# Kernel tuning notes

Hardware: AMD Instinct MI355X
Metric: run time of the kernel (lower is better)

Reference implementation:

```python
import jax, jax.numpy as jnp
import numpy as np

N_NODES = 100000


def _sage_conv(x, src, dst, Wl, b, Wr):
    """PyG SAGEConv with mean aggregation: lin_l(mean_{j->i} x_j) + lin_r(x_i)."""
    msg = x[src]  # [E, d] gather of source-node features
    s = jax.ops.segment_sum(msg, dst, num_segments=N_NODES)  # [N, d]
    deg = jax.ops.segment_sum(jnp.ones_like(dst, dtype=x.dtype), dst,
                              num_segments=N_NODES)  # [N]
    mean = s / jnp.maximum(deg, 1.0)[:, None]  # nodes with no in-edges -> 0
    return mean @ Wl.T + b + x @ Wr.T


def setup_inputs() -> dict:
    key = jax.random.key(0)
    ks = jax.random.split(key, 12)
    in_f, h_f, out_f = 64, 64, 32
    E_half = 800000
    x = jax.random.normal(ks[0], (N_NODES, in_f), dtype=jnp.float32)
    edge_index1 = jax.random.randint(ks[1], (2, E_half), 0, N_NODES, dtype=jnp.int64)
    edge_weight1 = jax.random.uniform(ks[2], (E_half,), dtype=jnp.float32)
    edge_index2 = jax.random.randint(ks[3], (2, E_half), 0, N_NODES, dtype=jnp.int64)
    edge_weight2 = jax.random.uniform(ks[4], (E_half,), dtype=jnp.float32)
    s1 = 1.0 / np.sqrt(in_f)
    s2 = 1.0 / np.sqrt(h_f)
    W1l = jax.random.uniform(ks[5], (h_f, in_f), minval=-s1, maxval=s1, dtype=jnp.float32)
    b1 = jax.random.uniform(ks[6], (h_f,), minval=-s1, maxval=s1, dtype=jnp.float32)
    W1r = jax.random.uniform(ks[7], (h_f, in_f), minval=-s1, maxval=s1, dtype=jnp.float32)
    W2l = jax.random.uniform(ks[8], (out_f, h_f), minval=-s2, maxval=s2, dtype=jnp.float32)
    b2 = jax.random.uniform(ks[9], (out_f,), minval=-s2, maxval=s2, dtype=jnp.float32)
    W2r = jax.random.uniform(ks[10], (out_f, h_f), minval=-s2, maxval=s2, dtype=jnp.float32)
    return {"x": x, "edge_index1": edge_index1, "edge_weight1": edge_weight1,
            "edge_index2": edge_index2, "edge_weight2": edge_weight2,
            "W1l": W1l, "b1": b1, "W1r": W1r, "W2l": W2l, "b2": b2, "W2r": W2r}


def reference(x, edge_index1, edge_weight1, edge_index2, edge_weight2,
              W1l, b1, W1r, W2l, b2, W2r):
    # concat adjacency lists (edge_weight is concatenated but unused by SAGEConv)
    edge_index = jnp.concatenate([edge_index1, edge_index2], axis=-1)
    _edge_weight = jnp.concatenate([edge_weight1, edge_weight2], axis=-1)  # unused
    src, dst = edge_index[0], edge_index[1]
    # F.dropout with training=False -> identity (eval-mode reference)
    h = _sage_conv(x, src, dst, W1l, b1, W1r)
    h = jax.nn.relu(h)
    out = _sage_conv(h, src, dst, W2l, b2, W2r)
    return out
```

## Files before the change

kernel.cpp:

```cpp
#include <hip/hip_runtime.h>


constexpr int N_NODES = 100000;
constexpr int E_HALF  = 800000;
constexpr int E_TOT   = 2 * E_HALF;
constexpr int CAP     = 64;
constexpr int OVF_CAP = 4096;
constexpr int NB      = 200;
constexpr int NPB     = 500;
constexpr int BCAP    = 12288;
constexpr int EPB_A   = 2048;
constexpr int EPT_A   = EPB_A / 256;

typedef short  s16x8 __attribute__((ext_vector_type(8)));
typedef float  f32x4 __attribute__((ext_vector_type(4)));
typedef unsigned short u16;

__device__ inline float bf(u16 u) { return __uint_as_float(((unsigned)u) << 16); }
__device__ inline u16 f2bf(float v) {
    unsigned b = __float_as_uint(v);
    b += 0x7FFFu + ((b >> 16) & 1u);
    return (u16)(b >> 16);
}
__device__ inline void acc4(float* s, uint2 v) {
    s[0] += __uint_as_float(v.x << 16);
    s[1] += __uint_as_float(v.x & 0xFFFF0000u);
    s[2] += __uint_as_float(v.y << 16);
    s[3] += __uint_as_float(v.y & 0xFFFF0000u);
}

__global__ __launch_bounds__(256) void binA_kernel(
    const int* __restrict__ ei1, const int* __restrict__ ei2,
    uint2* __restrict__ barr, int* __restrict__ bcur,
    int* __restrict__ ovfA_cnt, int* __restrict__ ovfA)
{
    __shared__ int   hist[NB], base[NB], cur[NB], lofs[NB];
    __shared__ int   scan[256];
    __shared__ int   aux[EPB_A];
    __shared__ uint2 staged[EPB_A];
    int tid = threadIdx.x;
    for (int t = tid; t < NB; t += 256) { hist[t] = 0; cur[t] = 0; }
    __syncthreads();

    int e0 = blockIdx.x * EPB_A;
    uint2 myE[EPT_A];
    int   myB[EPT_A];
    #pragma unroll
    for (int k = 0; k < EPT_A; k++) {
        int e = e0 + k * 256 + tid;
        myB[k] = -1;
        if (e < E_TOT) {
            const int* ei = (e < E_HALF) ? ei1 : ei2;
            int ee = (e < E_HALF) ? e : e - E_HALF;
            int dst = ei[E_HALF + ee];
            int src = ei[ee];
            myE[k] = make_uint2((unsigned)src, (unsigned)dst);
            myB[k] = dst / NPB;
            atomicAdd(&hist[myB[k]], 1);
        }
    }
    __syncthreads();

    int v = (tid < NB) ? hist[tid] : 0;
    scan[tid] = v;
    __syncthreads();
    #pragma unroll
    for (int off = 1; off < 256; off <<= 1) {
        int u = (tid >= off) ? scan[tid - off] : 0;
        __syncthreads();
        scan[tid] += u;
        __syncthreads();
    }
    if (tid < NB) lofs[tid] = scan[tid] - v;
    if (tid < NB) base[tid] = atomicAdd(&bcur[tid], hist[tid]);
    __syncthreads();

    #pragma unroll
    for (int k = 0; k < EPT_A; k++) {
        int b = myB[k];
        if (b < 0) continue;
        int rank = atomicAdd(&cur[b], 1);
        int p    = lofs[b] + rank;
        int gpos = base[b] + rank;
        if (gpos < BCAP) {
            staged[p] = myE[k];
            aux[p]    = b * BCAP + gpos;
        } else {
            aux[p] = -1;
            int o = atomicAdd(ovfA_cnt, 1);
            if (o < OVF_CAP) {
                ovfA[2 * o] = (int)myE[k].x; ovfA[2 * o + 1] = (int)myE[k].y;
            }
        }
    }
    __syncthreads();

    int tot = scan[255];
    for (int i = tid; i < tot; i += 256) {
        int a = aux[i];
        if (a >= 0) barr[a] = staged[i];
    }
}

__global__ __launch_bounds__(1024) void binB_kernel(
    const uint2* __restrict__ barr, const int* __restrict__ bcur,
    const int* __restrict__ ovfA_cnt, const int* __restrict__ ovfA,
    int* __restrict__ cnt, int* __restrict__ slots,
    int* __restrict__ ovfB_cnt, int* __restrict__ ovfB)
{
    __shared__ int lcnt[NPB];
    int tid = threadIdx.x, b = blockIdx.x;
    for (int t = tid; t < NPB; t += 1024) lcnt[t] = 0;
    __syncthreads();
    int nE = bcur[b]; if (nE > BCAP) nE = BCAP;
    int dbase = b * NPB;
    for (int i = tid; i < nE; i += 1024) {
        uint2 e = barr[b * BCAP + i];
        int dst = (int)e.y;
        int pos = atomicAdd(&lcnt[dst - dbase], 1);
        if (pos < CAP) {
            slots[dst * CAP + pos] = (int)e.x;
        } else {
            int o = atomicAdd(ovfB_cnt, 1);
            if (o < OVF_CAP) { ovfB[2 * o] = (int)e.x; ovfB[2 * o + 1] = dst; }
        }
    }
    __syncthreads();
    int nOA = *ovfA_cnt; if (nOA > OVF_CAP) nOA = OVF_CAP;
    for (int t = tid; t < nOA; t += 1024) {
        int src = ovfA[2 * t], dst = ovfA[2 * t + 1];
        if (dst >= dbase && dst < dbase + NPB) {
            int pos = atomicAdd(&lcnt[dst - dbase], 1);
            if (pos < CAP) {
                slots[dst * CAP + pos] = src;
            } else {
                int o = atomicAdd(ovfB_cnt, 1);
                if (o < OVF_CAP) { ovfB[2 * o] = src; ovfB[2 * o + 1] = dst; }
            }
        }
    }
    __syncthreads();
    for (int t = tid; t < NPB; t += 1024) {
        int n = dbase + t;
        if (n < N_NODES) cnt[n] = lcnt[t];
    }
}

__global__ __launch_bounds__(256) void prep_kernel(
    const float* __restrict__ x, u16* __restrict__ xb,
    const float* __restrict__ W1l, const float* __restrict__ W1r,
    const float* __restrict__ W2l, const float* __restrict__ W2r,
    short* __restrict__ B1hi, short* __restrict__ B1lo,
    short* __restrict__ B2hi, short* __restrict__ B2lo,
    int* __restrict__ zinit)
{
    int blk = blockIdx.x;
    if (blk == 6298) {
        for (int t = threadIdx.x; t < 320; t += 256) zinit[t] = 0;
        return;
    }
    if (blk < 6250) {
        int i = blk * 256 + threadIdx.x;
        float4 v = ((const float4*)x)[i];
        ushort4 rr;
        rr.x = f2bf(v.x); rr.y = f2bf(v.y); rr.z = f2bf(v.z); rr.w = f2bf(v.w);
        ((ushort4*)xb)[i] = rr;
        return;
    }
    int i = (blk - 6250) * 256 + threadIdx.x;
    float v; short* ph; short* pl; int idx;
    if (i < 64 * 128) {
        int o = i >> 7, k = i & 127;
        v = (k < 64) ? W1l[o * 64 + k] : W1r[o * 64 + (k - 64)];
        ph = B1hi; pl = B1lo; idx = i;
    } else {
        int j = i - 64 * 128;
        int o = j >> 6, k = j & 63;
        v = (o < 32) ? W2l[o * 64 + k] : W2r[(o - 32) * 64 + k];
        ph = B2hi; pl = B2lo; idx = j;
    }
    unsigned b  = __float_as_uint(v);
    float    hf = __uint_as_float(b & 0xFFFF0000u);
    float    r  = v - hf;
    ph[idx] = (short)(b >> 16);
    pl[idx] = (short)(__float_as_uint(r) >> 16);
}

__device__ inline void split8(float4 v0, float4 v1, s16x8& hi, s16x8& lo) {
    float vs[8] = {v0.x, v0.y, v0.z, v0.w, v1.x, v1.y, v1.z, v1.w};
    s16x8 h, l;
    #pragma unroll
    for (int j = 0; j < 8; j++) {
        unsigned b  = __float_as_uint(vs[j]);
        float    hf = __uint_as_float(b & 0xFFFF0000u);
        float    r  = vs[j] - hf;
        h[j] = (short)(b >> 16);
        l[j] = (short)(__float_as_uint(r) >> 16);
    }
    hi = h; lo = l;
}

template <int MT>
__global__ __launch_bounds__(256) void gather_gemm1_kernel(
    const u16*  __restrict__ xb,
    const float* __restrict__ x,
    const int*  __restrict__ cnt,
    const int*  __restrict__ slots,
    const int*  __restrict__ ovfB_cnt, const int* __restrict__ ovfB,
    const short* __restrict__ Bhi, const short* __restrict__ Blo,
    const float* __restrict__ bias, u16* __restrict__ hb)
{
    constexpr int RPW = MT * 16;
    __shared__ float ldsA[4][RPW][66];
    const int widx = threadIdx.x >> 6;
    const int lane = threadIdx.x & 63;
    const int m0   = (blockIdx.x * 4 + widx) * RPW;
    const int r = lane >> 4;
    const int c = lane & 15;

    int pdA, pdB, psvA, psvB;
    {
        int nA = m0, nB = m0 + 1;
        pdA  = (nA < N_NODES) ? cnt[nA] : 0;
        pdB  = (nB < N_NODES) ? cnt[nB] : 0;
        psvA = (nA < N_NODES) ? slots[nA * CAP + lane] : 0;
        psvB = (nB < N_NODES) ? slots[nB * CAP + lane] : 0;
    }
    #pragma unroll 1
    for (int j = 0; j < RPW; j += 2) {
        const int dA = pdA, dB = pdB;
        const int rsvA = psvA, rsvB = psvB;
        if (j + 2 < RPW) {
            int nA = m0 + j + 2, nB = m0 + j + 3;
            pdA  = (nA < N_NODES) ? cnt[nA] : 0;
            pdB  = (nB < N_NODES) ? cnt[nB] : 0;
            psvA = (nA < N_NODES) ? slots[nA * CAP + lane] : 0;
            psvB = (nB < N_NODES) ? slots[nB * CAP + lane] : 0;
        }
        const int cA = dA < CAP ? dA : CAP;
        const int cB = dB < CAP ? dB : CAP;
        const int svA = (lane < cA) ? rsvA : 0;
        const int svB = (lane < cB) ? rsvB : 0;
        float sA[16], sB[16];
        #pragma unroll
        for (int k = 0; k < 16; k++) { sA[k] = 0.f; sB[k] = 0.f; }
        const int cM = cA > cB ? cA : cB;
        for (int i = 0; i < cM; i += 16) {
            const int i0 = i + r, i1 = i + 4 + r, i2 = i + 8 + r, i3 = i + 12 + r;
            int tA0 = __shfl(svA, i0), tA1 = __shfl(svA, i1),
                tA2 = __shfl(svA, i2), tA3 = __shfl(svA, i3);
            int tB0 = __shfl(svB, i0), tB1 = __shfl(svB, i1),
                tB2 = __shfl(svB, i2), tB3 = __shfl(svB, i3);
            uint2 vA0 = make_uint2(0u, 0u), vA1 = vA0, vA2 = vA0, vA3 = vA0;
            uint2 vB0 = vA0, vB1 = vA0, vB2 = vA0, vB3 = vA0;
            if (i0 < cA) vA0 = *(const uint2*)&xb[tA0 * 64 + c * 4];
            if (i1 < cA) vA1 = *(const uint2*)&xb[tA1 * 64 + c * 4];
            if (i2 < cA) vA2 = *(const uint2*)&xb[tA2 * 64 + c * 4];
            if (i3 < cA) vA3 = *(const uint2*)&xb[tA3 * 64 + c * 4];
            if (i0 < cB) vB0 = *(const uint2*)&xb[tB0 * 64 + c * 4];
            if (i1 < cB) vB1 = *(const uint2*)&xb[tB1 * 64 + c * 4];
            if (i2 < cB) vB2 = *(const uint2*)&xb[tB2 * 64 + c * 4];
            if (i3 < cB) vB3 = *(const uint2*)&xb[tB3 * 64 + c * 4];
            acc4(&sA[0], vA0); acc4(&sA[4], vA1);
            acc4(&sA[8], vA2); acc4(&sA[12], vA3);
            acc4(&sB[0], vB0); acc4(&sB[4], vB1);
            acc4(&sB[8], vB2); acc4(&sB[12], vB3);
        }
        #pragma unroll
        for (int k = 0; k < 4; k++) {
            float fA = sA[k] + sA[k + 4] + sA[k + 8] + sA[k + 12];
            float fB = sB[k] + sB[k + 4] + sB[k + 8] + sB[k + 12];
            fA += __shfl_xor(fA, 16); fA += __shfl_xor(fA, 32);
            fB += __shfl_xor(fB, 16); fB += __shfl_xor(fB, 32);
            sA[k] = fA; sB[k] = fB;
        }
        if (r == 0) {
            const float rdA = 1.0f / fmaxf((float)dA, 1.0f);
            const float rdB = 1.0f / fmaxf((float)dB, 1.0f);
            float2* pA = (float2*)&ldsA[widx][j][c * 4];
            float2* pB = (float2*)&ldsA[widx][j + 1][c * 4];
            pA[0] = make_float2(sA[0] * rdA, sA[1] * rdA);
            pA[1] = make_float2(sA[2] * rdA, sA[3] * rdA);
            pB[0] = make_float2(sB[0] * rdB, sB[1] * rdB);
            pB[1] = make_float2(sB[2] * rdB, sB[3] * rdB);
        }
    }
    __syncthreads();

    {
        int nOv = *ovfB_cnt; if (nOv > OVF_CAP) nOv = OVF_CAP;
        for (int t = 0; t < nOv; ++t) {
            int src = ovfB[2 * t], dst = ovfB[2 * t + 1];
            if (dst >= m0 && dst < m0 + RPW && dst < N_NODES) {
                float rd = 1.0f / fmaxf((float)cnt[dst], 1.0f);
                ldsA[widx][dst - m0][lane] += bf(xb[src * 64 + lane]) * rd;
            }
        }
    }
    __syncthreads();

    f32x4 acc[MT][4];
    #pragma unroll
    for (int mt = 0; mt < MT; mt++)
        #pragma unroll
        for (int nt = 0; nt < 4; nt++) acc[mt][nt] = (f32x4)0.0f;

    #pragma unroll
    for (int half = 0; half < 2; half++) {
        #pragma unroll
        for (int sub = 0; sub < 2; sub++) {
            const int kf = sub * 32 + r * 8;
            const int kc = half * 64 + kf;
            s16x8 ahi[MT], alo[MT];
            #pragma unroll
            for (int mt = 0; mt < MT; mt++) {
                if (half == 0) {
                    const float2* p = (const float2*)&ldsA[widx][mt * 16 + c][kf];
                    float2 q0 = p[0], q1 = p[1], q2 = p[2], q3 = p[3];
                    split8(make_float4(q0.x, q0.y, q1.x, q1.y),
                           make_float4(q2.x, q2.y, q3.x, q3.y),
                           ahi[mt], alo[mt]);
                } else {
                    int row = m0 + mt * 16 + c;
                    row = row < N_NODES ? row : N_NODES - 1;
                    const float4* p = (const float4*)&x[row * 64 + kf];
                    split8(p[0], p[1], ahi[mt], alo[mt]);
                }
            }
            #pragma unroll
            for (int nt = 0; nt < 4; nt++) {
                const int n = nt * 16 + c;
                s16x8 bh = *(const s16x8*)&Bhi[n * 128 + kc];
                s16x8 bl = *(const s16x8*)&Blo[n * 128 + kc];
                #pragma unroll
                for (int mt = 0; mt < MT; mt++) {
                    acc[mt][nt] = __builtin_amdgcn_mfma_f32_16x16x32_bf16(ahi[mt], bh, acc[mt][nt], 0, 0, 0);
                    acc[mt][nt] = __builtin_amdgcn_mfma_f32_16x16x32_bf16(alo[mt], bh, acc[mt][nt], 0, 0, 0);
                    acc[mt][nt] = __builtin_amdgcn_mfma_f32_16x16x32_bf16(ahi[mt], bl, acc[mt][nt], 0, 0, 0);
                    acc[mt][nt] = __builtin_amdgcn_mfma_f32_16x16x32_bf16(alo[mt], bl, acc[mt][nt], 0, 0, 0);
                }
            }
        }
    }
    #pragma unroll
    for (int nt = 0; nt < 4; nt++) {
        float bv = bias[nt * 16 + c];
        #pragma unroll
        for (int mt = 0; mt < MT; mt++)
            #pragma unroll
            for (int rr = 0; rr < 4; rr++) {
                int row = m0 + mt * 16 + r * 4 + rr;
                if (row < N_NODES)
                    hb[row * 64 + nt * 16 + c] =
                        f2bf(fmaxf(acc[mt][nt][rr] + bv, 0.0f));
            }
    }
}

template <int MT>
__global__ __launch_bounds__(256) void gemm2_kernel(
    const u16* __restrict__ hb,
    const short* __restrict__ Bhi, const short* __restrict__ Blo,
    const float* __restrict__ b2,
    u16* __restrict__ y2b, float* __restrict__ z)
{
    int wave = (blockIdx.x * 256 + threadIdx.x) >> 6;
    int lane = threadIdx.x & 63;
    int m0   = wave * (MT * 16);
    if (m0 >= N_NODES) return;
    int quad = lane >> 4, l16 = lane & 15;

    f32x4 acc[MT][4];
    #pragma unroll
    for (int mt = 0; mt < MT; mt++)
        #pragma unroll
        for (int nt = 0; nt < 4; nt++) acc[mt][nt] = (f32x4)0.0f;

    #pragma unroll
    for (int sub = 0; sub < 2; sub++) {
        int kf = sub * 32 + quad * 8;
        s16x8 a[MT];
        #pragma unroll
        for (int mt = 0; mt < MT; mt++) {
            int row = m0 + mt * 16 + l16;
            row = row < N_NODES ? row : N_NODES - 1;
            a[mt] = *(const s16x8*)&hb[row * 64 + kf];
        }
        #pragma unroll
        for (int nt = 0; nt < 4; nt++) {
            int n = nt * 16 + l16;
            s16x8 bh = *(const s16x8*)&Bhi[n * 64 + kf];
            s16x8 bl = *(const s16x8*)&Blo[n * 64 + kf];
            #pragma unroll
            for (int mt = 0; mt < MT; mt++) {
                acc[mt][nt] = __builtin_amdgcn_mfma_f32_16x16x32_bf16(a[mt], bh, acc[mt][nt], 0, 0, 0);
                acc[mt][nt] = __builtin_amdgcn_mfma_f32_16x16x32_bf16(a[mt], bl, acc[mt][nt], 0, 0, 0);
            }
        }
    }
    #pragma unroll
    for (int nt = 0; nt < 4; nt++) {
        bool  isz = nt >= 2;
        int   col = (isz ? nt - 2 : nt) * 16 + l16;
        float bv  = isz ? b2[col] : 0.0f;
        #pragma unroll
        for (int mt = 0; mt < MT; mt++)
            #pragma unroll
            for (int r = 0; r < 4; r++) {
                int row = m0 + mt * 16 + quad * 4 + r;
                if (row < N_NODES) {
                    float v = acc[mt][nt][r] + bv;
                    if (isz) z[row * 32 + col] = v;
                    else     y2b[row * 32 + col] = f2bf(v);
                }
            }
    }
}

__global__ __launch_bounds__(256) void gather_mean32_kernel(
    const u16*  __restrict__ y2b,
    const float* __restrict__ z,
    const int*  __restrict__ cnt,
    const int*  __restrict__ slots,
    const int*  __restrict__ ovfB_cnt, const int* __restrict__ ovfB,
    float*      __restrict__ out)
{
    int node = blockIdx.x * 4 + (threadIdx.x >> 6);
    int lane = threadIdx.x & 63;
    int r    = lane >> 3;
    int c    = lane & 7;
    if (node >= N_NODES) return;
    int nOv = *ovfB_cnt; if (nOv > OVF_CAP) nOv = OVF_CAP;
    int cdeg = cnt[node];
    int cc   = cdeg < CAP ? cdeg : CAP;
    int slotv = (lane < cc) ? slots[node * CAP + lane] : 0;
    float s[16];
    #pragma unroll
    for (int k = 0; k < 16; k++) s[k] = 0.f;
    for (int i = 0; i < cc; i += 32) {
        int i0 = i + r, i1 = i + 8 + r, i2 = i + 16 + r, i3 = i + 24 + r;
        int t0 = __shfl(slotv, i0), t1 = __shfl(slotv, i1),
            t2 = __shfl(slotv, i2), t3 = __shfl(slotv, i3);
        uint2 v0 = make_uint2(0u, 0u), v1 = v0, v2 = v0, v3 = v0;
        if (i0 < cc) v0 = *(const uint2*)&y2b[t0 * 32 + c * 4];
        if (i1 < cc) v1 = *(const uint2*)&y2b[t1 * 32 + c * 4];
        if (i2 < cc) v2 = *(const uint2*)&y2b[t2 * 32 + c * 4];
        if (i3 < cc) v3 = *(const uint2*)&y2b[t3 * 32 + c * 4];
        acc4(&s[0], v0); acc4(&s[4], v1); acc4(&s[8], v2); acc4(&s[12], v3);
    }
    #pragma unroll
    for (int k = 0; k < 4; k++) {
        float f = s[k] + s[k + 4] + s[k + 8] + s[k + 12];
        f += __shfl_xor(f, 8); f += __shfl_xor(f, 16); f += __shfl_xor(f, 32);
        s[k] = f;
    }
    for (int t = 0; t < nOv; ++t) {
        int src = ovfB[2 * t], dst = ovfB[2 * t + 1];
        if (dst == node) {
            uint2 v = *(const uint2*)&y2b[src * 32 + c * 4];
            s[0] += __uint_as_float(v.x << 16);
            s[1] += __uint_as_float(v.x & 0xFFFF0000u);
            s[2] += __uint_as_float(v.y << 16);
            s[3] += __uint_as_float(v.y & 0xFFFF0000u);
        }
    }
    if (r == 0) {
        float rd = 1.0f / fmaxf((float)cdeg, 1.0f);
        float4 zz = *(const float4*)&z[node * 32 + c * 4];
        *(float4*)&out[node * 32 + c * 4] = make_float4(
            s[0] * rd + zz.x, s[1] * rd + zz.y,
            s[2] * rd + zz.z, s[3] * rd + zz.w);
    }
}

extern "C" void kernel_launch(void* const* d_in, const int* in_sizes, int n_in,
                              void* d_out, int out_size, void* d_ws, size_t ws_size,
                              hipStream_t stream) {
    const float* x   = (const float*)d_in[0];
    const int*   ei1 = (const int*)d_in[1];
    const int*   ei2 = (const int*)d_in[3];
    const float* W1l = (const float*)d_in[5];
    const float* b1  = (const float*)d_in[6];
    const float* W1r = (const float*)d_in[7];
    const float* W2l = (const float*)d_in[8];
    const float* b2  = (const float*)d_in[9];
    const float* W2r = (const float*)d_in[10];
    float* out = (float*)d_out;

    const size_t off_misc  = 400128;
    const size_t off_ovfAc = off_misc + 0;
    const size_t off_ovfBc = off_misc + 4;
    const size_t off_bcur  = off_misc + 256;
    const size_t off_ovfA  = off_misc + 1280;
    const size_t off_ovfB  = off_misc + 1280 + 8 * OVF_CAP;
    const size_t off_slots = 467200;
    const size_t off_m     = off_slots + (size_t)N_NODES * CAP * 4;
    const size_t off_h     = off_m + (size_t)N_NODES * 64 * 4;
    const size_t off_hb    = off_h + (size_t)N_NODES * 64 * 2;
    const size_t off_B1hi  = off_h + (size_t)N_NODES * 64 * 4;
    const size_t off_B1lo  = off_B1hi + 64 * 128 * 2;
    const size_t off_B2hi  = off_B1lo + 64 * 128 * 2;
    const size_t off_B2lo  = off_B2hi + 64 * 64 * 2;

    char*  ws     = (char*)d_ws;
    int*   cnt    = (int*)(ws + 0);
    int*   ovfA_c = (int*)(ws + off_ovfAc);
    int*   ovfB_c = (int*)(ws + off_ovfBc);
    int*   bcur   = (int*)(ws + off_bcur);
    int*   ovfA   = (int*)(ws + off_ovfA);
    int*   ovfB   = (int*)(ws + off_ovfB);
    int*   slots  = (int*)(ws + off_slots);
    uint2* barr   = (uint2*)(ws + off_m);
    u16*   xb     = (u16*)(ws + off_h);
    u16*   hb     = (u16*)(ws + off_hb);
    float* z      = (float*)(ws + off_m);
    u16*   y2b    = (u16*)(ws + off_m + (size_t)N_NODES * 32 * 4);
    short* B1hi   = (short*)(ws + off_B1hi);
    short* B1lo   = (short*)(ws + off_B1lo);
    short* B2hi   = (short*)(ws + off_B2hi);
    short* B2lo   = (short*)(ws + off_B2lo);

    prep_kernel<<<6250 + 48 + 1, 256, 0, stream>>>(
        x, xb, W1l, W1r, W2l, W2r, B1hi, B1lo, B2hi, B2lo,
        (int*)(ws + off_misc));

    binA_kernel<<<(E_TOT + EPB_A - 1) / EPB_A, 256, 0, stream>>>(
        ei1, ei2, barr, bcur, ovfA_c, ovfA);
    binB_kernel<<<NB, 1024, 0, stream>>>(
        barr, bcur, ovfA_c, ovfA, cnt, slots, ovfB_c, ovfB);

    {
        int waves  = (N_NODES + 31) / 32;
        int blocks = (waves + 3) / 4;
        gather_gemm1_kernel<2><<<blocks, 256, 0, stream>>>(
            xb, x, cnt, slots, ovfB_c, ovfB, B1hi, B1lo, b1, hb);
    }

    {
        int waves = (N_NODES + 63) / 64;
        gemm2_kernel<4><<<(waves + 3) / 4, 256, 0, stream>>>(
            hb, B2hi, B2lo, b2, y2b, z);
    }
    gather_mean32_kernel<<<N_NODES / 4, 256, 0, stream>>>(
        y2b, z, cnt, slots, ovfB_c, ovfB, out);
}
```

Measured before the change: 236.9 us.

## Fuse layer-2 GEMM into gather-GEMM1, fold bf16 conversion into binning kernel

Removes the separate prep and gemm2 kernels. The x-to-bf16 conversion now runs as extra blocks of the binning kernel, and the weight hi/lo bf16 split is done inline from fp32 weights inside the GEMMs. The hidden activations stay in LDS, so the second linear layer runs in the same kernel without writing hb to global memory. Counter zeroing moves to a memset. This saves launches and an HBM round-trip of h, at the cost of recomputing the weight splits in every wave and extra LDS syncs.

```diff
diff --git a/kernel.cpp b/kernel.cpp
--- a/kernel.cpp
+++ b/kernel.cpp
@@ -11,6 +11,8 @@
 constexpr int BCAP    = 12288;
 constexpr int EPB_A   = 2048;
 constexpr int EPT_A   = EPB_A / 256;
+constexpr int BINA_BLKS = (E_TOT + EPB_A - 1) / EPB_A;
+constexpr int CONV_BLKS = N_NODES * 64 / 4 / 256;
 
 typedef short  s16x8 __attribute__((ext_vector_type(8)));
 typedef float  f32x4 __attribute__((ext_vector_type(4)));
@@ -29,8 +31,23 @@
     s[3] += __uint_as_float(v.y & 0xFFFF0000u);
 }
 
+__device__ inline void split8(float4 v0, float4 v1, s16x8& hi, s16x8& lo) {
+    float vs[8] = {v0.x, v0.y, v0.z, v0.w, v1.x, v1.y, v1.z, v1.w};
+    s16x8 h, l;
+    #pragma unroll
+    for (int j = 0; j < 8; j++) {
+        unsigned b  = __float_as_uint(vs[j]);
+        float    hf = __uint_as_float(b & 0xFFFF0000u);
+        float    r  = vs[j] - hf;
+        h[j] = (short)(b >> 16);
+        l[j] = (short)(__float_as_uint(r) >> 16);
+    }
+    hi = h; lo = l;
+}
+
 __global__ __launch_bounds__(256) void binA_kernel(
     const int* __restrict__ ei1, const int* __restrict__ ei2,
+    const float* __restrict__ x, u16* __restrict__ xb,
     uint2* __restrict__ barr, int* __restrict__ bcur,
     int* __restrict__ ovfA_cnt, int* __restrict__ ovfA)
 {
@@ -39,6 +56,16 @@
     __shared__ int   aux[EPB_A];
     __shared__ uint2 staged[EPB_A];
     int tid = threadIdx.x;
+
+    if (blockIdx.x >= BINA_BLKS) {
+        int i = (blockIdx.x - BINA_BLKS) * 256 + tid;
+        float4 v = ((const float4*)x)[i];
+        ushort4 rr;
+        rr.x = f2bf(v.x); rr.y = f2bf(v.y); rr.z = f2bf(v.z); rr.w = f2bf(v.w);
+        ((ushort4*)xb)[i] = rr;
+        return;
+    }
+
     for (int t = tid; t < NB; t += 256) { hist[t] = 0; cur[t] = 0; }
     __syncthreads();
 
@@ -146,69 +173,18 @@
     }
 }
 
-__global__ __launch_bounds__(256) void prep_kernel(
-    const float* __restrict__ x, u16* __restrict__ xb,
-    const float* __restrict__ W1l, const float* __restrict__ W1r,
-    const float* __restrict__ W2l, const float* __restrict__ W2r,
-    short* __restrict__ B1hi, short* __restrict__ B1lo,
-    short* __restrict__ B2hi, short* __restrict__ B2lo,
-    int* __restrict__ zinit)
-{
-    int blk = blockIdx.x;
-    if (blk == 6298) {
-        for (int t = threadIdx.x; t < 320; t += 256) zinit[t] = 0;
-        return;
-    }
-    if (blk < 6250) {
-        int i = blk * 256 + threadIdx.x;
-        float4 v = ((const float4*)x)[i];
-        ushort4 rr;
-        rr.x = f2bf(v.x); rr.y = f2bf(v.y); rr.z = f2bf(v.z); rr.w = f2bf(v.w);
-        ((ushort4*)xb)[i] = rr;
-        return;
-    }
-    int i = (blk - 6250) * 256 + threadIdx.x;
-    float v; short* ph; short* pl; int idx;
-    if (i < 64 * 128) {
-        int o = i >> 7, k = i & 127;
-        v = (k < 64) ? W1l[o * 64 + k] : W1r[o * 64 + (k - 64)];
-        ph = B1hi; pl = B1lo; idx = i;
-    } else {
-        int j = i - 64 * 128;
-        int o = j >> 6, k = j & 63;
-        v = (o < 32) ? W2l[o * 64 + k] : W2r[(o - 32) * 64 + k];
-        ph = B2hi; pl = B2lo; idx = j;
-    }
-    unsigned b  = __float_as_uint(v);
-    float    hf = __uint_as_float(b & 0xFFFF0000u);
-    float    r  = v - hf;
-    ph[idx] = (short)(b >> 16);
-    pl[idx] = (short)(__float_as_uint(r) >> 16);
-}
-
-__device__ inline void split8(float4 v0, float4 v1, s16x8& hi, s16x8& lo) {
-    float vs[8] = {v0.x, v0.y, v0.z, v0.w, v1.x, v1.y, v1.z, v1.w};
-    s16x8 h, l;
-    #pragma unroll
-    for (int j = 0; j < 8; j++) {
-        unsigned b  = __float_as_uint(vs[j]);
-        float    hf = __uint_as_float(b & 0xFFFF0000u);
-        float    r  = vs[j] - hf;
-        h[j] = (short)(b >> 16);
-        l[j] = (short)(__float_as_uint(r) >> 16);
-    }
-    hi = h; lo = l;
-}
-
 template <int MT>
-__global__ __launch_bounds__(256) void gather_gemm1_kernel(
+__global__ __launch_bounds__(256) void gather_gemm12_kernel(
     const u16*  __restrict__ xb,
     const float* __restrict__ x,
     const int*  __restrict__ cnt,
     const int*  __restrict__ slots,
     const int*  __restrict__ ovfB_cnt, const int* __restrict__ ovfB,
-    const short* __restrict__ Bhi, const short* __restrict__ Blo,
-    const float* __restrict__ bias, u16* __restrict__ hb)
+    const float* __restrict__ W1l, const float* __restrict__ W1r,
+    const float* __restrict__ b1,
+    const float* __restrict__ W2l, const float* __restrict__ W2r,
+    const float* __restrict__ b2,
+    u16* __restrict__ y2b, float* __restrict__ z)
 {
     constexpr int RPW = MT * 16;
     __shared__ float ldsA[4][RPW][66];
@@ -217,6 +193,7 @@
     const int m0   = (blockIdx.x * 4 + widx) * RPW;
     const int r = lane >> 4;
     const int c = lane & 15;
+    u16* hbT = (u16*)&ldsA[widx][0][0];
 
     int pdA, pdB, psvA, psvB;
     {
@@ -247,10 +224,10 @@
         const int cM = cA > cB ? cA : cB;
         for (int i = 0; i < cM; i += 16) {
             const int i0 = i + r, i1 = i + 4 + r, i2 = i + 8 + r, i3 = i + 12 + r;
-            int tA0 = __shfl(svA, i0), tA1 = __shfl(svA, i1),
-                tA2 = __shfl(svA, i2), tA3 = __shfl(svA, i3);
-            int tB0 = __shfl(svB, i0), tB1 = __shfl(svB, i1),
-                tB2 = __shfl(svB, i2), tB3 = __shfl(svB, i3);
+            int tA0 = __shfl(svA, i0 & 63), tA1 = __shfl(svA, i1 & 63),
+                tA2 = __shfl(svA, i2 & 63), tA3 = __shfl(svA, i3 & 63);
+            int tB0 = __shfl(svB, i0 & 63), tB1 = __shfl(svB, i1 & 63),
+                tB2 = __shfl(svB, i2 & 63), tB3 = __shfl(svB, i3 & 63);
             uint2 vA0 = make_uint2(0u, 0u), vA1 = vA0, vA2 = vA0, vA3 = vA0;
             uint2 vB0 = vA0, vB1 = vA0, vB2 = vA0, vB3 = vA0;
             if (i0 < cA) vA0 = *(const uint2*)&xb[tA0 * 64 + c * 4];
@@ -261,9 +238,9 @@
             if (i1 < cB) vB1 = *(const uint2*)&xb[tB1 * 64 + c * 4];
             if (i2 < cB) vB2 = *(const uint2*)&xb[tB2 * 64 + c * 4];
             if (i3 < cB) vB3 = *(const uint2*)&xb[tB3 * 64 + c * 4];
-            acc4(&sA[0], vA0); acc4(&sA[4], vA1);
+            acc4(&sA[0], vA0); acc4(&sA[4],  vA1);
             acc4(&sA[8], vA2); acc4(&sA[12], vA3);
-            acc4(&sB[0], vB0); acc4(&sB[4], vB1);
+            acc4(&sB[0], vB0); acc4(&sB[4],  vB1);
             acc4(&sB[8], vB2); acc4(&sB[12], vB3);
         }
         #pragma unroll
@@ -307,10 +284,10 @@
 
     #pragma unroll
     for (int half = 0; half < 2; half++) {
+        const float* W1 = half ? W1r : W1l;
         #pragma unroll
         for (int sub = 0; sub < 2; sub++) {
             const int kf = sub * 32 + r * 8;
-            const int kc = half * 64 + kf;
             s16x8 ahi[MT], alo[MT];
             #pragma unroll
             for (int mt = 0; mt < MT; mt++) {
@@ -330,8 +307,9 @@
             #pragma unroll
             for (int nt = 0; nt < 4; nt++) {
                 const int n = nt * 16 + c;
-                s16x8 bh = *(const s16x8*)&Bhi[n * 128 + kc];
-                s16x8 bl = *(const s16x8*)&Blo[n * 128 + kc];
+                const float4* wp = (const float4*)&W1[n * 64 + kf];
+                s16x8 bh, bl;
+                split8(wp[0], wp[1], bh, bl);
                 #pragma unroll
                 for (int mt = 0; mt < MT; mt++) {
                     acc[mt][nt] = __builtin_amdgcn_mfma_f32_16x16x32_bf16(ahi[mt], bh, acc[mt][nt], 0, 0, 0);
@@ -342,74 +320,62 @@
             }
         }
     }
+    __syncthreads();
+
     #pragma unroll
     for (int nt = 0; nt < 4; nt++) {
-        float bv = bias[nt * 16 + c];
+        float bv = b1[nt * 16 + c];
+        #pragma unroll
+        for (int mt = 0; mt < MT; mt++)
+            #pragma unroll
+            for (int rr = 0; rr < 4; rr++) {
+                int lrow = mt * 16 + r * 4 + rr;
+                u16 hv = (m0 + lrow < N_NODES)
+                           ? f2bf(fmaxf(acc[mt][nt][rr] + bv, 0.0f)) : (u16)0;
+                hbT[lrow * 72 + nt * 16 + c] = hv;
+            }
+    }
+    __syncthreads();
+
+    f32x4 acc2[MT][4];
+    #pragma unroll
+    for (int mt = 0; mt < MT; mt++)
+        #pragma unroll
+        for (int nt = 0; nt < 4; nt++) acc2[mt][nt] = (f32x4)0.0f;
+
+    #pragma unroll
+    for (int sub = 0; sub < 2; sub++) {
+        const int kf = sub * 32 + r * 8;
+        s16x8 a2[MT];
+        #pragma unroll
+        for (int mt = 0; mt < MT; mt++)
+            a2[mt] = *(const s16x8*)&hbT[(mt * 16 + c) * 72 + kf];
+        #pragma unroll
+        for (int nt = 0; nt < 4; nt++) {
+            const int n = nt * 16 + c;
+            const float4* wp = (n < 32) ? (const float4*)&W2l[n * 64 + kf]
+                                        : (const float4*)&W2r[(n - 32) * 64 + kf];
+            s16x8 bh, bl;
+            split8(wp[0], wp[1], bh, bl);
+            #pragma unroll
+            for (int mt = 0; mt < MT; mt++) {
+                acc2[mt][nt] = __builtin_amdgcn_mfma_f32_16x16x32_bf16(a2[mt], bh, acc2[mt][nt], 0, 0, 0);
+                acc2[mt][nt] = __builtin_amdgcn_mfma_f32_16x16x32_bf16(a2[mt], bl, acc2[mt][nt], 0, 0, 0);
+            }
+        }
+    }
+    #pragma unroll
+    for (int nt = 0; nt < 4; nt++) {
+        bool  isz = nt >= 2;
+        int   col = (isz ? nt - 2 : nt) * 16 + c;
+        float bv  = isz ? b2[col] : 0.0f;
         #pragma unroll
         for (int mt = 0; mt < MT; mt++)
             #pragma unroll
             for (int rr = 0; rr < 4; rr++) {
                 int row = m0 + mt * 16 + r * 4 + rr;
-                if (row < N_NODES)
-                    hb[row * 64 + nt * 16 + c] =
-                        f2bf(fmaxf(acc[mt][nt][rr] + bv, 0.0f));
-            }
-    }
-}
-
-template <int MT>
-__global__ __launch_bounds__(256) void gemm2_kernel(
-    const u16* __restrict__ hb,
-    const short* __restrict__ Bhi, const short* __restrict__ Blo,
-    const float* __restrict__ b2,
-    u16* __restrict__ y2b, float* __restrict__ z)
-{
-    int wave = (blockIdx.x * 256 + threadIdx.x) >> 6;
-    int lane = threadIdx.x & 63;
-    int m0   = wave * (MT * 16);
-    if (m0 >= N_NODES) return;
-    int quad = lane >> 4, l16 = lane & 15;
-
-    f32x4 acc[MT][4];
-    #pragma unroll
-    for (int mt = 0; mt < MT; mt++)
-        #pragma unroll
-        for (int nt = 0; nt < 4; nt++) acc[mt][nt] = (f32x4)0.0f;
-
-    #pragma unroll
-    for (int sub = 0; sub < 2; sub++) {
-        int kf = sub * 32 + quad * 8;
-        s16x8 a[MT];
-        #pragma unroll
-        for (int mt = 0; mt < MT; mt++) {
-            int row = m0 + mt * 16 + l16;
-            row = row < N_NODES ? row : N_NODES - 1;
-            a[mt] = *(const s16x8*)&hb[row * 64 + kf];
-        }
-        #pragma unroll
-        for (int nt = 0; nt < 4; nt++) {
-            int n = nt * 16 + l16;
-            s16x8 bh = *(const s16x8*)&Bhi[n * 64 + kf];
-            s16x8 bl = *(const s16x8*)&Blo[n * 64 + kf];
-            #pragma unroll
-            for (int mt = 0; mt < MT; mt++) {
-                acc[mt][nt] = __builtin_amdgcn_mfma_f32_16x16x32_bf16(a[mt], bh, acc[mt][nt], 0, 0, 0);
-                acc[mt][nt] = __builtin_amdgcn_mfma_f32_16x16x32_bf16(a[mt], bl, acc[mt][nt], 0, 0, 0);
-            }
-        }
-    }
-    #pragma unroll
-    for (int nt = 0; nt < 4; nt++) {
-        bool  isz = nt >= 2;
-        int   col = (isz ? nt - 2 : nt) * 16 + l16;
-        float bv  = isz ? b2[col] : 0.0f;
-        #pragma unroll
-        for (int mt = 0; mt < MT; mt++)
-            #pragma unroll
-            for (int r = 0; r < 4; r++) {
-                int row = m0 + mt * 16 + quad * 4 + r;
                 if (row < N_NODES) {
-                    float v = acc[mt][nt][r] + bv;
+                    float v = acc2[mt][nt][rr] + bv;
                     if (isz) z[row * 32 + col] = v;
                     else     y2b[row * 32 + col] = f2bf(v);
                 }
@@ -496,11 +462,6 @@
     const size_t off_slots = 467200;
     const size_t off_m     = off_slots + (size_t)N_NODES * CAP * 4;
     const size_t off_h     = off_m + (size_t)N_NODES * 64 * 4;
-    const size_t off_hb    = off_h + (size_t)N_NODES * 64 * 2;
-    const size_t off_B1hi  = off_h + (size_t)N_NODES * 64 * 4;
-    const size_t off_B1lo  = off_B1hi + 64 * 128 * 2;
-    const size_t off_B2hi  = off_B1lo + 64 * 128 * 2;
-    const size_t off_B2lo  = off_B2hi + 64 * 64 * 2;
 
     char*  ws     = (char*)d_ws;
     int*   cnt    = (int*)(ws + 0);
@@ -512,35 +473,24 @@
     int*   slots  = (int*)(ws + off_slots);
     uint2* barr   = (uint2*)(ws + off_m);
     u16*   xb     = (u16*)(ws + off_h);
-    u16*   hb     = (u16*)(ws + off_hb);
     float* z      = (float*)(ws + off_m);
     u16*   y2b    = (u16*)(ws + off_m + (size_t)N_NODES * 32 * 4);
-    short* B1hi   = (short*)(ws + off_B1hi);
-    short* B1lo   = (short*)(ws + off_B1lo);
-    short* B2hi   = (short*)(ws + off_B2hi);
-    short* B2lo   = (short*)(ws + off_B2lo);
-
-    prep_kernel<<<6250 + 48 + 1, 256, 0, stream>>>(
-        x, xb, W1l, W1r, W2l, W2r, B1hi, B1lo, B2hi, B2lo,
-        (int*)(ws + off_misc));
-
-    binA_kernel<<<(E_TOT + EPB_A - 1) / EPB_A, 256, 0, stream>>>(
-        ei1, ei2, barr, bcur, ovfA_c, ovfA);
+
+    hipMemsetAsync(ws + off_misc, 0, 1280, stream);
+
+    binA_kernel<<<BINA_BLKS + CONV_BLKS, 256, 0, stream>>>(
+        ei1, ei2, x, xb, barr, bcur, ovfA_c, ovfA);
     binB_kernel<<<NB, 1024, 0, stream>>>(
         barr, bcur, ovfA_c, ovfA, cnt, slots, ovfB_c, ovfB);
 
     {
         int waves  = (N_NODES + 31) / 32;
         int blocks = (waves + 3) / 4;
-        gather_gemm1_kernel<2><<<blocks, 256, 0, stream>>>(
-            xb, x, cnt, slots, ovfB_c, ovfB, B1hi, B1lo, b1, hb);
-    }
-
-    {
-        int waves = (N_NODES + 63) / 64;
-        gemm2_kernel<4><<<(waves + 3) / 4, 256, 0, stream>>>(
-            hb, B2hi, B2lo, b2, y2b, z);
-    }
+        gather_gemm12_kernel<2><<<blocks, 256, 0, stream>>>(
+            xb, x, cnt, slots, ovfB_c, ovfB,
+            W1l, W1r, b1, W2l, W2r, b2, y2b, z);
+    }
+
     gather_mean32_kernel<<<N_NODES / 4, 256, 0, stream>>>(
         y2b, z, cnt, slots, ovfB_c, ovfB, out);
 }
```

Result: slower. 252.0 us (+6.4%).
